# Kernel optimization log

Measured on AMD Instinct MI355X. Metric: run time of the kernel, lower is better.

The kernel has to match this reference:

```python
import jax, jax.numpy as jnp
import numpy as np

N_USERS = 50000
N_ITEMS = 30000
NNZ = 1_600_000
EMBED = 128
ATT = 128
TAU = 0.5


def setup_inputs() -> dict:
    key = jax.random.key(0)
    ks = jax.random.split(key, 9)
    user_embed = jax.random.normal(ks[0], (N_USERS, EMBED), dtype=jnp.float32)
    item_embed = jax.random.normal(ks[1], (N_ITEMS, EMBED), dtype=jnp.float32)
    Wq = jax.random.normal(ks[2], (ATT, EMBED), dtype=jnp.float32) * (1.0 / np.sqrt(EMBED))
    bq = jnp.zeros((ATT,), dtype=jnp.float32)
    Wk = jax.random.normal(ks[3], (ATT, EMBED), dtype=jnp.float32) * (1.0 / np.sqrt(EMBED))
    bk = jnp.zeros((ATT,), dtype=jnp.float32)
    adj_vals = jnp.ones((NNZ,), dtype=jnp.float32)
    gumbel_u_ui = jax.random.uniform(ks[4], (NNZ,), dtype=jnp.float32, minval=1e-10, maxval=1.0)
    gumbel_u_iu = jax.random.uniform(ks[5], (NNZ,), dtype=jnp.float32, minval=1e-10, maxval=1.0)
    rows = jax.random.randint(ks[6], (NNZ,), 0, N_USERS, dtype=jnp.int32)
    cols = jax.random.randint(ks[7], (NNZ,), 0, N_ITEMS, dtype=jnp.int32)
    return dict(user_embed=user_embed, item_embed=item_embed, Wq=Wq, bq=bq, Wk=Wk, bk=bk,
                adj_vals=adj_vals, gumbel_u_ui=gumbel_u_ui, gumbel_u_iu=gumbel_u_iu,
                rows=rows, cols=cols)


def _segment_softmax(vals, seg, num_segments):
    # numerically stable softmax over edges grouped by segment id (sparse row softmax)
    m = jax.ops.segment_max(vals, seg, num_segments=num_segments)
    e = jnp.exp(vals - m[seg])
    s = jax.ops.segment_sum(e, seg, num_segments=num_segments)
    return e / s[seg]


def reference(user_embed, item_embed, Wq, bq, Wk, bk, adj_vals, gumbel_u_ui, gumbel_u_iu, rows, cols):
    # ---- M_ui = sparse_softmax_rows( (adj * (Q(u) @ K(i).T) - G) / tau ) on edge support ----
    Qu = user_embed @ Wq.T + bq          # [U, A]
    Ki = item_embed @ Wk.T + bk          # [I, A]
    # edge-wise dot: equals dense (Qu @ Ki.T)[rows, cols] without materializing [U, I]
    w_ui = adj_vals * jnp.einsum('ed,ed->e', Qu[rows], Ki[cols])
    g_ui = jnp.log(-jnp.log(gumbel_u_ui))
    ui_vals = _segment_softmax((w_ui - g_ui) / TAU, rows, N_USERS)
    # ---- M_iu: transpose adjacency, Q over items, K over users, row-softmax over items ----
    Qi = item_embed @ Wq.T + bq          # [I, A]
    Ku = user_embed @ Wk.T + bk          # [U, A]
    w_iu = adj_vals * jnp.einsum('ed,ed->e', Qi[cols], Ku[rows])
    g_iu = jnp.log(-jnp.log(gumbel_u_iu))
    iu_vals = _segment_softmax((w_iu - g_iu) / TAU, cols, N_ITEMS)
    # block mask [[0, M_ui], [M_iu, 0]]: pads contribute nothing, so the nonzero
    # values of the concatenated mask are exactly these two edge-value arrays.
    return jnp.stack([ui_vals, iu_vals])  # [2, NNZ]
```

## Files before the change

kernel.cpp:

```cpp
#include <hip/hip_runtime.h>
#include <hip/hip_bf16.h>


#define EMB 128
#define TAUINV 2.0f
#define LOG2E 1.44269504f
#define CAP 128
#define OCAP 65536

__device__ __forceinline__ unsigned fkey(float f) {
    unsigned u = __float_as_uint(f);
    return (u & 0x80000000u) ? ~u : (u | 0x80000000u);
}
__device__ __forceinline__ float fdecode(unsigned u) {
    return __uint_as_float((u & 0x80000000u) ? (u ^ 0x80000000u) : ~u);
}

__device__ __forceinline__ double dexp_fast(float lg) {
    float t = lg * LOG2E;
    float kf = floorf(t);
    float f = exp2f(t - kf);
    return ldexp((double)f, (int)kf);
}

__global__ void k_prep(const float* __restrict__ Wq, const float* __restrict__ Wk,
                       const float* __restrict__ bq, const float* __restrict__ bk,
                       float* __restrict__ BIGM, float* __restrict__ v1,
                       float* __restrict__ v2, float* __restrict__ c0) {
    int e1 = blockIdx.x, e2 = threadIdx.x;
    float acc = 0.f;
    for (int a = 0; a < EMB; ++a) acc += Wq[a * EMB + e1] * Wk[a * EMB + e2];
    BIGM[e2 * 256 + e1] = acc;
    BIGM[e1 * 256 + 128 + e2] = acc;
    if (e2 == 0) { float s = 0.f; for (int a = 0; a < EMB; ++a) s += Wq[a * EMB + e1] * bk[a]; v1[e1] = s; }
    if (e2 == 1) { float s = 0.f; for (int a = 0; a < EMB; ++a) s += Wk[a * EMB + e1] * bq[a]; v2[e1] = s; }
    if (e1 == 0 && e2 == 2) { float s = 0.f; for (int a = 0; a < EMB; ++a) s += bq[a] * bk[a]; c0[0] = s; }
    if (e1 == 0 && e2 == 3) { float s = 0.f; for (int a = 0; a < EMB; ++a) s += fabsf(bq[a]) + fabsf(bk[a]); c0[1] = s; }
}

__global__ __launch_bounds__(256) void k_cd(const float* __restrict__ Xi,
                                            const float* __restrict__ BIGM,
                                            float* __restrict__ CD, int nItems) {
    __shared__ float Xs[32][EMB];
    __shared__ float Ms[32][256];
    const int t = threadIdx.x;
    const int m0 = blockIdx.x * 32;

    const float4* Xi4 = (const float4*)Xi;
    float4* Xs4 = (float4*)Xs;
    for (int idx = t; idx < 32 * 32; idx += 256) {
        int r = idx >> 5, c = idx & 31;
        int row = m0 + r;
        Xs4[idx] = (row < nItems) ? Xi4[(size_t)row * 32 + c]
                                  : make_float4(0.f, 0.f, 0.f, 0.f);
    }

    const int tc = t & 63;
    const int tr = t >> 6;
    float4 acc[8] = {};

    const float4* BG4 = (const float4*)BIGM;
    float4* Ms4 = (float4*)Ms;
    for (int kc = 0; kc < EMB; kc += 32) {
        __syncthreads();
        for (int idx = t; idx < 32 * 64; idx += 256)
            Ms4[idx] = BG4[(size_t)(kc + (idx >> 6)) * 64 + (idx & 63)];
        __syncthreads();
#pragma unroll
        for (int kk = 0; kk < 32; ++kk) {
            float4 w = Ms4[kk * 64 + tc];
#pragma unroll
            for (int i = 0; i < 8; ++i) {
                float x = Xs[tr * 8 + i][kc + kk];
                acc[i].x += x * w.x; acc[i].y += x * w.y;
                acc[i].z += x * w.z; acc[i].w += x * w.w;
            }
        }
    }
#pragma unroll
    for (int i = 0; i < 8; ++i) {
        int row = m0 + tr * 8 + i;
        if (row < nItems)
            ((float4*)(CD + (size_t)row * 256))[tc] = acc[i];
    }
}

__global__ void k_rowdot2(const float* __restrict__ Xu, const float* __restrict__ Xi,
                          int U, int I,
                          const float* __restrict__ v1, const float* __restrict__ v2,
                          float2* __restrict__ t12, float2* __restrict__ u12) {
    int g = blockIdx.x * 8 + (threadIdx.x >> 5);
    int l = threadIdx.x & 31;
    if (g >= U + I) return;
    const float* X = (g < U) ? (Xu + (size_t)g * EMB) : (Xi + (size_t)(g - U) * EMB);
    float4 x = ((const float4*)X)[l];
    float4 av = ((const float4*)v1)[l];
    float4 bv = ((const float4*)v2)[l];
    float pa = x.x * av.x + x.y * av.y + x.z * av.z + x.w * av.w;
    float pb = x.x * bv.x + x.y * bv.y + x.z * bv.z + x.w * bv.w;
    for (int off = 16; off; off >>= 1) { pa += __shfl_xor(pa, off); pb += __shfl_xor(pb, off); }
    if (l == 0) {
        if (g < U) t12[g] = make_float2(pa, pb);
        else       u12[g - U] = make_float2(pb, pa);
    }
}

__global__ void k_scatter_fc(const int* __restrict__ rows, const int* __restrict__ cols,
                             const float* __restrict__ adj, const float* __restrict__ gu1,
                             const float* __restrict__ gu2,
                             const float2* __restrict__ t12, const float2* __restrict__ u12,
                             const float* __restrict__ c0p, int nnz,
                             unsigned* __restrict__ cnt, int4* __restrict__ SA,
                             float* __restrict__ SB, int* __restrict__ OV,
                             unsigned* __restrict__ ovfc) {
    const float c0 = c0p[0];
    const bool useb = (c0p[1] != 0.f);
    int i = blockIdx.x * blockDim.x + threadIdx.x, st = gridDim.x * blockDim.x;
    for (int e = i; e < nnz; e += st) {
        int r = rows[e], c = cols[e];
        unsigned pos = atomicAdd(&cnt[c], 1u);
        float a = adj[e];
        float g1 = logf(-logf(gu1[e]));
        float g2 = logf(-logf(gu2[e]));
        float b1 = -g1 * TAUINV;
        float b2 = -g2 * TAUINV;
        if (useb) {
            float2 tt = t12[r];
            float2 uu = u12[c];
            b1 += a * (tt.x + uu.x + c0) * TAUINV;
            b2 += a * (tt.y + uu.y + c0) * TAUINV;
        }
        if (pos < CAP) {
            size_t s = (size_t)c * CAP + pos;
            SA[s] = make_int4(r, e, __float_as_int(a * TAUINV), __float_as_int(b1));
            SB[s] = b2;
        } else {
            unsigned o = atomicAdd(ovfc, 1u);
            if (o < OCAP) {
                int* p = OV + (size_t)o * 6;
                p[0] = r; p[1] = c; p[2] = e;
                p[3] = __float_as_int(a * TAUINV);
                p[4] = __float_as_int(b1); p[5] = __float_as_int(b2);
            }
        }
    }
}

__global__ __launch_bounds__(256) void k_edge14(
    const float* __restrict__ Xu, const float* __restrict__ CD,
    const unsigned* __restrict__ cnt, const int4* __restrict__ SA,
    const float* __restrict__ SB,
    float2* __restrict__ L12, double* __restrict__ s1d, double* __restrict__ s2d,
    int I) {
    const int g = threadIdx.x >> 4, l = threadIdx.x & 15;
    const int c = blockIdx.x * 16 + g;
    if (c >= I) return;
    unsigned n = cnt[c]; if (n > CAP) n = CAP;
    if (n == 0) return;
    const unsigned lo = (unsigned)c * CAP;
    const unsigned hi = lo + n;
    const float4* cd = (const float4*)(CD + (size_t)c * 256);
    const float4 cv0 = cd[l], cv1 = cd[l + 16];
    const float4 dv0 = cd[l + 32], dv1 = cd[l + 48];
    double s2acc = 0.0;
    for (unsigned j = lo; j < hi; ++j) {
        int4 m = SA[j];
        float b2s = SB[j];
        const float4* xu = (const float4*)(Xu + (size_t)m.x * EMB);
        float4 x0 = xu[l], x1 = xu[l + 16];
        float p1 = x0.x * cv0.x + x0.y * cv0.y + x0.z * cv0.z + x0.w * cv0.w
                 + x1.x * cv1.x + x1.y * cv1.y + x1.z * cv1.z + x1.w * cv1.w;
        float p2 = x0.x * dv0.x + x0.y * dv0.y + x0.z * dv0.z + x0.w * dv0.w
                 + x1.x * dv1.x + x1.y * dv1.y + x1.z * dv1.z + x1.w * dv1.w;
#pragma unroll
        for (int off = 1; off < 16; off <<= 1) {
            p1 += __shfl_xor(p1, off);
            p2 += __shfl_xor(p2, off);
        }
        if (l < 2) {
            float aP = __int_as_float(m.z);
            float bP = (l == 0) ? __int_as_float(m.w) : b2s;
            float lg = fmaf(aP, (l == 0) ? p1 : p2, bP);
            double ev = dexp_fast(lg);
            ((float*)(L12 + m.y))[l] = lg;
            if (l == 0) unsafeAtomicAdd(s1d + m.x, ev);
            else        s2acc += ev;
        }
    }
    if (l == 1) s2d[c] = s2acc;
}

__global__ void k_ovf(const float* __restrict__ Xu, const float* __restrict__ CD,
                      const int* __restrict__ OV, const unsigned* __restrict__ ovfc,
                      float2* __restrict__ L12, double* __restrict__ s1d,
                      double* __restrict__ s2d) {
    int n = (int)*ovfc; if (n > OCAP) n = OCAP;
    if (n == 0) return;
    const int gid = (blockIdx.x * blockDim.x + threadIdx.x) >> 4;
    const int ng = (gridDim.x * blockDim.x) >> 4;
    const int l = threadIdx.x & 15;
    for (int i = gid; i < n; i += ng) {
        const int* p = OV + (size_t)i * 6;
        int r = p[0], c = p[1], e = p[2];
        const float4* xu = (const float4*)(Xu + (size_t)r * EMB);
        const float4* cd = (const float4*)(CD + (size_t)c * 256);
        float4 x0 = xu[l], x1 = xu[l + 16];
        float4 cv0 = cd[l], cv1 = cd[l + 16];
        float4 dv0 = cd[l + 32], dv1 = cd[l + 48];
        float p1 = x0.x * cv0.x + x0.y * cv0.y + x0.z * cv0.z + x0.w * cv0.w
                 + x1.x * cv1.x + x1.y * cv1.y + x1.z * cv1.z + x1.w * cv1.w;
        float p2 = x0.x * dv0.x + x0.y * dv0.y + x0.z * dv0.z + x0.w * dv0.w
                 + x1.x * dv1.x + x1.y * dv1.y + x1.z * dv1.z + x1.w * dv1.w;
#pragma unroll
        for (int off = 1; off < 16; off <<= 1) {
            p1 += __shfl_xor(p1, off);
            p2 += __shfl_xor(p2, off);
        }
        if (l < 2) {
            float aP = __int_as_float(p[3]);
            float bP = __int_as_float((l == 0) ? p[4] : p[5]);
            float lg = fmaf(aP, (l == 0) ? p1 : p2, bP);
            double ev = dexp_fast(lg);
            ((float*)(L12 + e))[l] = lg;
            if (l == 0) unsafeAtomicAdd(s1d + r, ev);
            else        unsafeAtomicAdd(s2d + c, ev);
        }
    }
}

__global__ void k_ls(const double* __restrict__ s1d, const double* __restrict__ s2d,
                     float* __restrict__ ls1, float* __restrict__ ls2, int U, int I) {
    int i = blockIdx.x * blockDim.x + threadIdx.x;
    if (i >= U + I) return;
    double s = (i < U) ? s1d[i] : s2d[i - U];
    int ex;
    double m = frexp(s, &ex);
    float l2 = log2f((float)m) + (float)ex;
    if (i < U) ls1[i] = l2; else ls2[i - U] = l2;
}

__global__ void k_fin4(const int* __restrict__ rows, const int* __restrict__ cols,
                       const float2* __restrict__ L12,
                       const float* __restrict__ ls1, const float* __restrict__ ls2,
                       float* __restrict__ out, int nnz) {
    int i = blockIdx.x * blockDim.x + threadIdx.x, st = gridDim.x * blockDim.x;
    for (int e = i; e < nnz; e += st) {
        float2 lg = L12[e];
        out[e]       = exp2f(fmaf(lg.x, LOG2E, -ls1[rows[e]]));
        out[nnz + e] = exp2f(fmaf(lg.y, LOG2E, -ls2[cols[e]]));
    }
}

__global__ __launch_bounds__(256) void k_edge1(
    const float* __restrict__ Xu, const float* __restrict__ CD,
    const float2* __restrict__ t12, const float2* __restrict__ u12,
    const float* __restrict__ c0p, const float* __restrict__ adj,
    const float* __restrict__ gu1, const float* __restrict__ gu2,
    const int* __restrict__ rows, const int* __restrict__ cols,
    float* __restrict__ L1, float* __restrict__ L2,
    unsigned* __restrict__ mx1, unsigned* __restrict__ mx2, int nnz) {
    const int gid = blockIdx.x * 8 + (threadIdx.x >> 5);
    const int l = threadIdx.x & 31;
    const int stride = gridDim.x * 8;
    const float c0 = c0p[0];
    for (int e = gid; e < nnz; e += stride) {
        int r = rows[e], c = cols[e];
        float4 xu = ((const float4*)(Xu + (size_t)r * EMB))[l];
        const float4* cd = (const float4*)(CD + (size_t)c * 256);
        float4 cv = cd[l];
        float4 dv = cd[32 + l];
        float p1 = xu.x * cv.x + xu.y * cv.y + xu.z * cv.z + xu.w * cv.w;
        float p2 = xu.x * dv.x + xu.y * dv.y + xu.z * dv.z + xu.w * dv.w;
        for (int off = 16; off; off >>= 1) { p1 += __shfl_xor(p1, off); p2 += __shfl_xor(p2, off); }
        if (l < 2) {
            float p = (l == 0) ? p1 : p2;
            float2 tt = t12[r];
            float2 uu = u12[c];
            float tb = (l == 0) ? tt.x : tt.y;
            float ub = (l == 0) ? uu.x : uu.y;
            float g = logf(-logf(((l == 0) ? gu1 : gu2)[e]));
            float w = adj[e] * (p + tb + ub + c0);
            float lg = (w - g) * TAUINV;
            if (l == 0) { L1[e] = lg; atomicMax(mx1 + r, fkey(lg)); }
            else        { L2[e] = lg; atomicMax(mx2 + c, fkey(lg)); }
        }
    }
}

__global__ void k_sum(const int* __restrict__ rows, const int* __restrict__ cols,
                      const float* __restrict__ L1, const float* __restrict__ L2,
                      const unsigned* __restrict__ mx1, const unsigned* __restrict__ mx2,
                      float* __restrict__ s1, float* __restrict__ s2, int nnz) {
    int i = blockIdx.x * blockDim.x + threadIdx.x, st = gridDim.x * blockDim.x;
    for (int e = i; e < nnz; e += st) {
        int r = rows[e], c = cols[e];
        atomicAdd(s1 + r, expf(L1[e] - fdecode(mx1[r])));
        atomicAdd(s2 + c, expf(L2[e] - fdecode(mx2[c])));
    }
}

__global__ void k_fin2(const int* __restrict__ rows, const int* __restrict__ cols,
                       const float* __restrict__ L1, const float* __restrict__ L2,
                       const unsigned* __restrict__ mx1, const unsigned* __restrict__ mx2,
                       const float* __restrict__ s1, const float* __restrict__ s2,
                       float* __restrict__ out, int nnz) {
    int i = blockIdx.x * blockDim.x + threadIdx.x, st = gridDim.x * blockDim.x;
    for (int e = i; e < nnz; e += st) {
        int r = rows[e], c = cols[e];
        out[e]       = expf(L1[e] - fdecode(mx1[r])) / s1[r];
        out[nnz + e] = expf(L2[e] - fdecode(mx2[c])) / s2[c];
    }
}

extern "C" void kernel_launch(void* const* d_in, const int* in_sizes, int n_in,
                              void* d_out, int out_size, void* d_ws, size_t ws_size,
                              hipStream_t stream) {
    const float* Xu  = (const float*)d_in[0];
    const float* Xi  = (const float*)d_in[1];
    const float* Wq  = (const float*)d_in[2];
    const float* bq  = (const float*)d_in[3];
    const float* Wk  = (const float*)d_in[4];
    const float* bk  = (const float*)d_in[5];
    const float* adj = (const float*)d_in[6];
    const float* gu1 = (const float*)d_in[7];
    const float* gu2 = (const float*)d_in[8];
    const int* rows  = (const int*)d_in[9];
    const int* cols  = (const int*)d_in[10];
    float* out = (float*)d_out;

    const int U   = in_sizes[0] / EMB;
    const int I   = in_sizes[1] / EMB;
    const int nnz = in_sizes[6];

    char* w = (char*)d_ws;
    size_t off_b = 0;
    auto alloc = [&](size_t bytes) {
        char* p = w + off_b;
        off_b += (bytes + 15) & ~(size_t)15;
        return p;
    };

    float* BIGM = (float*)alloc(32768 * 4);
    float* v1   = (float*)alloc(128 * 4);
    float* v2   = (float*)alloc(128 * 4);
    float* c0   = (float*)alloc(64 * 4);
    float2* t12 = (float2*)alloc((size_t)U * 8);
    float2* u12 = (float2*)alloc((size_t)I * 8);
    float* CD   = (float*)alloc((size_t)I * 256 * 4);
    float2* L12 = (float2*)alloc((size_t)nnz * 8);
    size_t base_need = off_b;
    double* s1d    = (double*)alloc((size_t)U * 8);
    unsigned* cnt  = (unsigned*)alloc((size_t)I * 4);
    unsigned* ovfc = (unsigned*)alloc(16 * 4);
    double* s2d    = (double*)alloc((size_t)I * 8);
    float* ls1     = (float*)alloc((size_t)U * 4);
    float* ls2     = (float*)alloc((size_t)I * 4);
    int4* SA = (int4*)alloc((size_t)I * CAP * 16);
    float* SB = (float*)alloc((size_t)I * CAP * 4);
    int* OV = (int*)alloc((size_t)OCAP * 24);
    size_t sorted_need = off_b;
    unsigned* mx1 = (unsigned*)alloc((size_t)U * 4);
    unsigned* mx2 = (unsigned*)alloc((size_t)I * 4);
    float* s1f  = (float*)alloc((size_t)U * 4);
    float* s2f  = (float*)alloc((size_t)I * 4);
    size_t fallback_need = off_b;

    const bool use_sorted = (sorted_need <= ws_size);
    if (!use_sorted && fallback_need > ws_size) return;

    k_prep<<<128, 128, 0, stream>>>(Wq, Wk, bq, bk, BIGM, v1, v2, c0);
    k_cd<<<(I + 31) / 32, 256, 0, stream>>>(Xi, BIGM, CD, I);
    k_rowdot2<<<(U + I + 7) / 8, 256, 0, stream>>>(Xu, Xi, U, I, v1, v2, t12, u12);

    if (use_sorted) {
        (void)hipMemsetAsync(s1d, 0, (size_t)U * 8 + (size_t)I * 4 + 64, stream);
        k_scatter_fc<<<2048, 256, 0, stream>>>(rows, cols, adj, gu1, gu2,
                                               t12, u12, c0, nnz, cnt, SA, SB,
                                               OV, ovfc);
        k_edge14<<<(I + 15) / 16, 256, 0, stream>>>(Xu, CD, cnt, SA, SB, L12,
                                                    s1d, s2d, I);
        k_ovf<<<64, 256, 0, stream>>>(Xu, CD, OV, ovfc, L12, s1d, s2d);
        k_ls<<<(U + I + 255) / 256, 256, 0, stream>>>(s1d, s2d, ls1, ls2, U, I);
        k_fin4<<<2048, 256, 0, stream>>>(rows, cols, L12, ls1, ls2, out, nnz);
    } else {
        float* L1 = (float*)L12;
        float* L2 = L1 + nnz;
        (void)hipMemsetAsync(mx1, 0, (size_t)(2 * (U + I)) * 4, stream);
        k_edge1<<<4096, 256, 0, stream>>>(Xu, CD, t12, u12, c0, adj, gu1, gu2,
                                          rows, cols, L1, L2, mx1, mx2, nnz);
        k_sum<<<2048, 256, 0, stream>>>(rows, cols, L1, L2, mx1, mx2, s1f, s2f, nnz);
        k_fin2<<<2048, 256, 0, stream>>>(rows, cols, L1, L2, mx1, mx2, s1f, s2f,
                                         out, nnz);
    }
}
```

Measured before the change: 388.4 us.

## Fuse CD GEMM and edge scatter into one kernel with block-range split

Merges the item-side CD matrix product and the edge scatter/bucketing pass into a single launch. The first nbCD blocks compute CD tiles and the remaining blocks do the scatter, so the compute-bound GEMM and the atomic, memory-bound scatter can run concurrently on different CUs and one launch gap disappears. The fused kernel reserves the GEMM's shared-memory footprint for every block, including the scatter blocks that do not use it, which may lower occupancy for the scatter work. The fallback path keeps a separate k_cd launch.

```diff
diff --git a/kernel.cpp b/kernel.cpp
--- a/kernel.cpp
+++ b/kernel.cpp
@@ -7,6 +7,7 @@
 #define LOG2E 1.44269504f
 #define CAP 128
 #define OCAP 65536
+#define NSCAT 2048
 
 __device__ __forceinline__ unsigned fkey(float f) {
     unsigned u = __float_as_uint(f);
@@ -36,53 +37,6 @@
     if (e2 == 1) { float s = 0.f; for (int a = 0; a < EMB; ++a) s += Wk[a * EMB + e1] * bq[a]; v2[e1] = s; }
     if (e1 == 0 && e2 == 2) { float s = 0.f; for (int a = 0; a < EMB; ++a) s += bq[a] * bk[a]; c0[0] = s; }
     if (e1 == 0 && e2 == 3) { float s = 0.f; for (int a = 0; a < EMB; ++a) s += fabsf(bq[a]) + fabsf(bk[a]); c0[1] = s; }
-}
-
-__global__ __launch_bounds__(256) void k_cd(const float* __restrict__ Xi,
-                                            const float* __restrict__ BIGM,
-                                            float* __restrict__ CD, int nItems) {
-    __shared__ float Xs[32][EMB];
-    __shared__ float Ms[32][256];
-    const int t = threadIdx.x;
-    const int m0 = blockIdx.x * 32;
-
-    const float4* Xi4 = (const float4*)Xi;
-    float4* Xs4 = (float4*)Xs;
-    for (int idx = t; idx < 32 * 32; idx += 256) {
-        int r = idx >> 5, c = idx & 31;
-        int row = m0 + r;
-        Xs4[idx] = (row < nItems) ? Xi4[(size_t)row * 32 + c]
-                                  : make_float4(0.f, 0.f, 0.f, 0.f);
-    }
-
-    const int tc = t & 63;
-    const int tr = t >> 6;
-    float4 acc[8] = {};
-
-    const float4* BG4 = (const float4*)BIGM;
-    float4* Ms4 = (float4*)Ms;
-    for (int kc = 0; kc < EMB; kc += 32) {
-        __syncthreads();
-        for (int idx = t; idx < 32 * 64; idx += 256)
-            Ms4[idx] = BG4[(size_t)(kc + (idx >> 6)) * 64 + (idx & 63)];
-        __syncthreads();
-#pragma unroll
-        for (int kk = 0; kk < 32; ++kk) {
-            float4 w = Ms4[kk * 64 + tc];
-#pragma unroll
-            for (int i = 0; i < 8; ++i) {
-                float x = Xs[tr * 8 + i][kc + kk];
-                acc[i].x += x * w.x; acc[i].y += x * w.y;
-                acc[i].z += x * w.z; acc[i].w += x * w.w;
-            }
-        }
-    }
-#pragma unroll
-    for (int i = 0; i < 8; ++i) {
-        int row = m0 + tr * 8 + i;
-        if (row < nItems)
-            ((float4*)(CD + (size_t)row * 256))[tc] = acc[i];
-    }
 }
 
 __global__ void k_rowdot2(const float* __restrict__ Xu, const float* __restrict__ Xi,
@@ -105,42 +59,91 @@
     }
 }
 
-__global__ void k_scatter_fc(const int* __restrict__ rows, const int* __restrict__ cols,
-                             const float* __restrict__ adj, const float* __restrict__ gu1,
-                             const float* __restrict__ gu2,
-                             const float2* __restrict__ t12, const float2* __restrict__ u12,
-                             const float* __restrict__ c0p, int nnz,
-                             unsigned* __restrict__ cnt, int4* __restrict__ SA,
-                             float* __restrict__ SB, int* __restrict__ OV,
-                             unsigned* __restrict__ ovfc) {
-    const float c0 = c0p[0];
-    const bool useb = (c0p[1] != 0.f);
-    int i = blockIdx.x * blockDim.x + threadIdx.x, st = gridDim.x * blockDim.x;
-    for (int e = i; e < nnz; e += st) {
-        int r = rows[e], c = cols[e];
-        unsigned pos = atomicAdd(&cnt[c], 1u);
-        float a = adj[e];
-        float g1 = logf(-logf(gu1[e]));
-        float g2 = logf(-logf(gu2[e]));
-        float b1 = -g1 * TAUINV;
-        float b2 = -g2 * TAUINV;
-        if (useb) {
-            float2 tt = t12[r];
-            float2 uu = u12[c];
-            b1 += a * (tt.x + uu.x + c0) * TAUINV;
-            b2 += a * (tt.y + uu.y + c0) * TAUINV;
-        }
-        if (pos < CAP) {
-            size_t s = (size_t)c * CAP + pos;
-            SA[s] = make_int4(r, e, __float_as_int(a * TAUINV), __float_as_int(b1));
-            SB[s] = b2;
-        } else {
-            unsigned o = atomicAdd(ovfc, 1u);
-            if (o < OCAP) {
-                int* p = OV + (size_t)o * 6;
-                p[0] = r; p[1] = c; p[2] = e;
-                p[3] = __float_as_int(a * TAUINV);
-                p[4] = __float_as_int(b1); p[5] = __float_as_int(b2);
+__global__ __launch_bounds__(256) void k_mid(
+    const float* __restrict__ Xi, const float* __restrict__ BIGM,
+    float* __restrict__ CD, int nItems, int nbCD,
+    const int* __restrict__ rows, const int* __restrict__ cols,
+    const float* __restrict__ adj, const float* __restrict__ gu1,
+    const float* __restrict__ gu2,
+    const float2* __restrict__ t12, const float2* __restrict__ u12,
+    const float* __restrict__ c0p, int nnz,
+    unsigned* __restrict__ cnt, int4* __restrict__ SA,
+    float* __restrict__ SB, int* __restrict__ OV,
+    unsigned* __restrict__ ovfc) {
+    __shared__ float Xs[32][EMB];
+    __shared__ float Ms[32][256];
+    if (blockIdx.x < (unsigned)nbCD) {
+        const int t = threadIdx.x;
+        const int m0 = blockIdx.x * 32;
+
+        const float4* Xi4 = (const float4*)Xi;
+        float4* Xs4 = (float4*)Xs;
+        for (int idx = t; idx < 32 * 32; idx += 256) {
+            int r = idx >> 5, c = idx & 31;
+            int row = m0 + r;
+            Xs4[idx] = (row < nItems) ? Xi4[(size_t)row * 32 + c]
+                                      : make_float4(0.f, 0.f, 0.f, 0.f);
+        }
+
+        const int tc = t & 63;
+        const int tr = t >> 6;
+        float4 acc[8] = {};
+
+        const float4* BG4 = (const float4*)BIGM;
+        float4* Ms4 = (float4*)Ms;
+        for (int kc = 0; kc < EMB; kc += 32) {
+            __syncthreads();
+            for (int idx = t; idx < 32 * 64; idx += 256)
+                Ms4[idx] = BG4[(size_t)(kc + (idx >> 6)) * 64 + (idx & 63)];
+            __syncthreads();
+#pragma unroll
+            for (int kk = 0; kk < 32; ++kk) {
+                float4 w = Ms4[kk * 64 + tc];
+#pragma unroll
+                for (int i = 0; i < 8; ++i) {
+                    float x = Xs[tr * 8 + i][kc + kk];
+                    acc[i].x += x * w.x; acc[i].y += x * w.y;
+                    acc[i].z += x * w.z; acc[i].w += x * w.w;
+                }
+            }
+        }
+#pragma unroll
+        for (int i = 0; i < 8; ++i) {
+            int row = m0 + tr * 8 + i;
+            if (row < nItems)
+                ((float4*)(CD + (size_t)row * 256))[tc] = acc[i];
+        }
+    } else {
+        const float c0 = c0p[0];
+        const bool useb = (c0p[1] != 0.f);
+        int i = (blockIdx.x - nbCD) * blockDim.x + threadIdx.x;
+        int st = NSCAT * blockDim.x;
+        for (int e = i; e < nnz; e += st) {
+            int r = rows[e], c = cols[e];
+            unsigned pos = atomicAdd(&cnt[c], 1u);
+            float a = adj[e];
+            float g1 = logf(-logf(gu1[e]));
+            float g2 = logf(-logf(gu2[e]));
+            float b1 = -g1 * TAUINV;
+            float b2 = -g2 * TAUINV;
+            if (useb) {
+                float2 tt = t12[r];
+                float2 uu = u12[c];
+                b1 += a * (tt.x + uu.x + c0) * TAUINV;
+                b2 += a * (tt.y + uu.y + c0) * TAUINV;
+            }
+            if (pos < CAP) {
+                size_t s = (size_t)c * CAP + pos;
+                SA[s] = make_int4(r, e, __float_as_int(a * TAUINV), __float_as_int(b1));
+                SB[s] = b2;
+            } else {
+                unsigned o = atomicAdd(ovfc, 1u);
+                if (o < OCAP) {
+                    int* p = OV + (size_t)o * 6;
+                    p[0] = r; p[1] = c; p[2] = e;
+                    p[3] = __float_as_int(a * TAUINV);
+                    p[4] = __float_as_int(b1); p[5] = __float_as_int(b2);
+                }
             }
         }
     }
@@ -248,6 +251,50 @@
         float2 lg = L12[e];
         out[e]       = exp2f(fmaf(lg.x, LOG2E, -ls1[rows[e]]));
         out[nnz + e] = exp2f(fmaf(lg.y, LOG2E, -ls2[cols[e]]));
+    }
+}
+
+__global__ __launch_bounds__(256) void k_cd(const float* __restrict__ Xi,
+                                            const float* __restrict__ BIGM,
+                                            float* __restrict__ CD, int nItems) {
+    __shared__ float Xs[32][EMB];
+    __shared__ float Ms[32][256];
+    const int t = threadIdx.x;
+    const int m0 = blockIdx.x * 32;
+    const float4* Xi4 = (const float4*)Xi;
+    float4* Xs4 = (float4*)Xs;
+    for (int idx = t; idx < 32 * 32; idx += 256) {
+        int r = idx >> 5, c = idx & 31;
+        int row = m0 + r;
+        Xs4[idx] = (row < nItems) ? Xi4[(size_t)row * 32 + c]
+                                  : make_float4(0.f, 0.f, 0.f, 0.f);
+    }
+    const int tc = t & 63;
+    const int tr = t >> 6;
+    float4 acc[8] = {};
+    const float4* BG4 = (const float4*)BIGM;
+    float4* Ms4 = (float4*)Ms;
+    for (int kc = 0; kc < EMB; kc += 32) {
+        __syncthreads();
+        for (int idx = t; idx < 32 * 64; idx += 256)
+            Ms4[idx] = BG4[(size_t)(kc + (idx >> 6)) * 64 + (idx & 63)];
+        __syncthreads();
+#pragma unroll
+        for (int kk = 0; kk < 32; ++kk) {
+            float4 w = Ms4[kk * 64 + tc];
+#pragma unroll
+            for (int i = 0; i < 8; ++i) {
+                float x = Xs[tr * 8 + i][kc + kk];
+                acc[i].x += x * w.x; acc[i].y += x * w.y;
+                acc[i].z += x * w.z; acc[i].w += x * w.w;
+            }
+        }
+    }
+#pragma unroll
+    for (int i = 0; i < 8; ++i) {
+        int row = m0 + tr * 8 + i;
+        if (row < nItems)
+            ((float4*)(CD + (size_t)row * 256))[tc] = acc[i];
     }
 }
 
@@ -331,6 +378,7 @@
     const int U   = in_sizes[0] / EMB;
     const int I   = in_sizes[1] / EMB;
     const int nnz = in_sizes[6];
+    const int nbCD = (I + 31) / 32;
 
     char* w = (char*)d_ws;
     size_t off_b = 0;
@@ -369,14 +417,14 @@
     if (!use_sorted && fallback_need > ws_size) return;
 
     k_prep<<<128, 128, 0, stream>>>(Wq, Wk, bq, bk, BIGM, v1, v2, c0);
-    k_cd<<<(I + 31) / 32, 256, 0, stream>>>(Xi, BIGM, CD, I);
     k_rowdot2<<<(U + I + 7) / 8, 256, 0, stream>>>(Xu, Xi, U, I, v1, v2, t12, u12);
 
     if (use_sorted) {
         (void)hipMemsetAsync(s1d, 0, (size_t)U * 8 + (size_t)I * 4 + 64, stream);
-        k_scatter_fc<<<2048, 256, 0, stream>>>(rows, cols, adj, gu1, gu2,
-                                               t12, u12, c0, nnz, cnt, SA, SB,
-                                               OV, ovfc);
+        k_mid<<<nbCD + NSCAT, 256, 0, stream>>>(Xi, BIGM, CD, I, nbCD,
+                                                rows, cols, adj, gu1, gu2,
+                                                t12, u12, c0, nnz, cnt, SA, SB,
+                                                OV, ovfc);
         k_edge14<<<(I + 15) / 16, 256, 0, stream>>>(Xu, CD, cnt, SA, SB, L12,
                                                     s1d, s2d, I);
         k_ovf<<<64, 256, 0, stream>>>(Xu, CD, OV, ovfc, L12, s1d, s2d);
@@ -386,6 +434,7 @@
         float* L1 = (float*)L12;
         float* L2 = L1 + nnz;
         (void)hipMemsetAsync(mx1, 0, (size_t)(2 * (U + I)) * 4, stream);
+        k_cd<<<nbCD, 256, 0, stream>>>(Xi, BIGM, CD, I);
         k_edge1<<<4096, 256, 0, stream>>>(Xu, CD, t12, u12, c0, adj, gu1, gu2,
                                           rows, cols, L1, L2, mx1, mx2, nnz);
         k_sum<<<2048, 256, 0, stream>>>(rows, cols, L1, L2, mx1, mx2, s1f, s2f, nnz);
```

Result: faster. 359.0 us (-7.6%).
